# Performance work log

Hardware: AMD Instinct MI355X
Metric: run time of the kernel (lower is better)

The kernel has to match this reference:

```python
import jax, jax.numpy as jnp
import numpy as np


def _conv1x1(x, w, b):
    # x: (B,C,H,W), w: (O,C), b: (O,)
    return jnp.einsum('oc,bchw->bohw', w, x) + b[None, :, None, None]


def _avg_pool2(x):
    B, C, H, W = x.shape
    return x.reshape(B, C, H // 2, 2, W // 2, 2).mean(axis=(3, 5))


def setup_inputs() -> dict:
    key = jax.random.key(0)
    B, C, H, W = 8, 64, 64, 64
    ks = jax.random.split(key, 14)
    s = 1.0 / np.sqrt(C)

    def wb(k1, k2):
        return (jax.random.uniform(k1, (C, C), jnp.float32, -s, s),
                jax.random.uniform(k2, (C,), jnp.float32, -s, s))

    w_q, b_q = wb(ks[0], ks[1])
    w_K, b_K = wb(ks[2], ks[3])
    w_V, b_V = wb(ks[4], ks[5])
    w_Q, b_Q = wb(ks[6], ks[7])
    w_k, b_k = wb(ks[8], ks[9])
    w_v, b_v = wb(ks[10], ks[11])
    x = jax.random.normal(ks[12], (B, C, H, W), jnp.float32)
    gamma = jnp.ones((1,), jnp.float32)
    return dict(x=x, w_q=w_q, b_q=b_q, w_K=w_K, b_K=b_K, w_V=w_V, b_V=b_V,
                w_Q=w_Q, b_Q=b_Q, w_k=w_k, b_k=b_k, w_v=w_v, b_v=b_v,
                gamma=gamma)


def reference(x, w_q, b_q, w_K, b_K, w_V, b_V, w_Q, b_Q, w_k, b_k, w_v, b_v, gamma):
    B, C, H, W = x.shape
    N = H * W
    N4 = N // 4

    # Stage 1: pooled queries vs full key/value
    q = _conv1x1(x, w_q, b_q)                      # (B,C,H,W); torch views as (B,C,W,H) but H==W
    qp = _avg_pool2(q).reshape(B, C, N4).transpose(0, 2, 1)   # (B,N/4,C)
    Kf = _conv1x1(x, w_K, b_K).reshape(B, C, N)                # (B,C,N)
    Vf = _conv1x1(x, w_V, b_V).reshape(B, C, N)                # (B,C,N)
    attn = jax.nn.softmax(jnp.einsum('bnc,bcm->bnm', qp, Kf), axis=-1)  # (B,N/4,N)
    out = jnp.einsum('bcm,bnm->bcn', Vf, attn)                 # (B,C,N/4)
    out = out.reshape(B, C, H // 2, W // 2)

    # Stage 2: full queries vs pooled-derived key/value
    Qf = _conv1x1(x, w_Q, b_Q).reshape(B, C, N).transpose(0, 2, 1)  # (B,N,C)
    kp = _conv1x1(out, w_k, b_k).reshape(B, C, N4)                  # (B,C,N/4)
    vp = _conv1x1(out, w_v, b_v).reshape(B, C, N4)                  # (B,C,N/4)
    attn2 = jax.nn.softmax(jnp.einsum('bnc,bcm->bnm', Qf, kp), axis=-1)  # (B,N,N/4)
    out2 = jnp.einsum('bcm,bnm->bcn', vp, attn2).reshape(B, C, H, W)

    return gamma * out2 + x
```

## Files before the change

kernel.cpp:

```cpp
#include <hip/hip_runtime.h>
#include <math.h>


typedef __bf16 bf16;
typedef __attribute__((ext_vector_type(4))) __bf16 bf16x4;
typedef __attribute__((ext_vector_type(8))) __bf16 bf16x8;
typedef __attribute__((ext_vector_type(4))) float f32x4;

__global__ __launch_bounds__(256) void transpool_kernel(const float* __restrict__ x,
                                                        bf16* __restrict__ xT,
                                                        bf16* __restrict__ xpT) {
    __shared__ float tile[128 * 65];
    const int t  = threadIdx.x;
    const int h2 = blockIdx.x;
    const int b  = blockIdx.y;
    const int n0 = h2 * 128;
    #pragma unroll
    for (int i = 0; i < 32; ++i) {
        int lin = i * 256 + t;
        int n = lin & 127, c = lin >> 7;
        tile[n * 65 + c] = x[((size_t)b * 64 + c) * 4096 + n0 + n];
    }
    __syncthreads();
    #pragma unroll
    for (int i = 0; i < 4; ++i) {
        int slot = i * 256 + t;
        int n = slot >> 3, c0 = (slot & 7) * 8;
        bf16 tmp[8];
        #pragma unroll
        for (int j = 0; j < 8; ++j) tmp[j] = (bf16)tile[n * 65 + c0 + j];
        *(bf16x8*)(xT + ((size_t)b * 4096 + n0 + n) * 64 + c0) = *(bf16x8*)tmp;
    }
    {
        int wp = t & 31, c0 = (t >> 5) * 8;
        bf16 tmp[8];
        #pragma unroll
        for (int j = 0; j < 8; ++j) {
            float a = tile[(2 * wp) * 65 + c0 + j] + tile[(2 * wp + 1) * 65 + c0 + j]
                    + tile[(64 + 2 * wp) * 65 + c0 + j] + tile[(64 + 2 * wp + 1) * 65 + c0 + j];
            tmp[j] = (bf16)(0.25f * a);
        }
        *(bf16x8*)(xpT + ((size_t)b * 1024 + h2 * 32 + wp) * 64 + c0) = *(bf16x8*)tmp;
    }
}

__global__ __launch_bounds__(256) void proj_all_kernel(
    const bf16* __restrict__ xT, const bf16* __restrict__ xpT,
    const float* __restrict__ w_K, const float* __restrict__ b_K, bf16* __restrict__ Kt,
    const float* __restrict__ w_Q, const float* __restrict__ b_Q, bf16* __restrict__ Qt,
    const float* __restrict__ w_V, const float* __restrict__ b_V, bf16* __restrict__ Vf,
    const float* __restrict__ w_q, const float* __restrict__ b_q, bf16* __restrict__ qpt)
{
    const int z = blockIdx.z;
    if (z == 3 && blockIdx.x >= 4) return;
    const bf16*  XT = (z == 3) ? xpT : xT;
    const int    N  = (z == 3) ? 1024 : 4096;
    const float* W  = (z == 0) ? w_K : (z == 1) ? w_Q : (z == 2) ? w_V : w_q;
    const float* Bs = (z == 0) ? b_K : (z == 1) ? b_Q : (z == 2) ? b_V : b_q;
    bf16*        Y  = (z == 0) ? Kt  : (z == 1) ? Qt  : (z == 2) ? Vf  : qpt;
    const int    tr = (z == 2) ? 0 : 1;

    const int lane = threadIdx.x & 63;
    const int w    = threadIdx.x >> 6;
    const int c16 = lane & 15, q4 = lane >> 4;
    const int n0 = (blockIdx.x * 4 + w) * 64;
    const int b  = blockIdx.y;

    bf16x8 wa[4][2];
    #pragma unroll
    for (int to = 0; to < 4; ++to)
        #pragma unroll
        for (int h = 0; h < 2; ++h) {
            const float* wp = W + (16 * to + c16) * 64 + q4 * 8 + 32 * h;
            float4 f0 = *(const float4*)wp;
            float4 f1 = *(const float4*)(wp + 4);
            bf16 tmp[8] = {(bf16)f0.x, (bf16)f0.y, (bf16)f0.z, (bf16)f0.w,
                           (bf16)f1.x, (bf16)f1.y, (bf16)f1.z, (bf16)f1.w};
            wa[to][h] = *(bf16x8*)tmp;
        }

    f32x4 acc[4][4];
    #pragma unroll
    for (int to = 0; to < 4; ++to)
        #pragma unroll
        for (int tn = 0; tn < 4; ++tn) acc[to][tn] = (f32x4){0.f, 0.f, 0.f, 0.f};

    #pragma unroll
    for (int tn = 0; tn < 4; ++tn) {
        const bf16* xrow = XT + ((size_t)b * N + n0 + 16 * tn + c16) * 64 + q4 * 8;
        bf16x8 xb0 = *(const bf16x8*)xrow;
        bf16x8 xb1 = *(const bf16x8*)(xrow + 32);
        #pragma unroll
        for (int to = 0; to < 4; ++to) {
            acc[to][tn] = __builtin_amdgcn_mfma_f32_16x16x32_bf16(wa[to][0], xb0, acc[to][tn], 0, 0, 0);
            acc[to][tn] = __builtin_amdgcn_mfma_f32_16x16x32_bf16(wa[to][1], xb1, acc[to][tn], 0, 0, 0);
        }
    }

    #pragma unroll
    for (int to = 0; to < 4; ++to) {
        float4 b4 = *(const float4*)(Bs + 16 * to + q4 * 4);
        float bias[4] = {b4.x, b4.y, b4.z, b4.w};
        #pragma unroll
        for (int tn = 0; tn < 4; ++tn) {
            if (tr) {
                bf16 yv[4];
                #pragma unroll
                for (int r = 0; r < 4; ++r) yv[r] = (bf16)(acc[to][tn][r] + bias[r]);
                *(bf16x4*)(Y + ((size_t)b * N + n0 + 16 * tn + c16) * 64 + 16 * to + q4 * 4) = *(bf16x4*)yv;
            } else {
                #pragma unroll
                for (int r = 0; r < 4; ++r)
                    Y[((size_t)b * 64 + 16 * to + q4 * 4 + r) * N + n0 + 16 * tn + c16] =
                        (bf16)(acc[to][tn][r] + bias[r]);
            }
        }
    }
}

template<int NSPLIT, int PLAYOUT>
__global__ __launch_bounds__(256) void flash_kernel(
    const bf16* __restrict__ Qt, const bf16* __restrict__ Kt,
    const bf16* __restrict__ Vn, int NQ, int L,
    float* __restrict__ Opart, float* __restrict__ Mbuf, float* __restrict__ Lbuf)
{
    const int tid  = threadIdx.x;
    const int lane = tid & 63;
    const int w    = tid >> 6;
    const int c16  = lane & 15;
    const int q4   = lane >> 4;
    const int b    = blockIdx.y;
    const int n0   = blockIdx.x * 128 + w * 32;
    const int s    = blockIdx.z;
    const int SL   = L / NSPLIT;
    const int k0   = s * SL;
    const int ntiles = SL / 64;

    __shared__ __align__(16) bf16 Ks[2][64 * 72];
    __shared__ __align__(16) bf16 Vs[2][64 * 72];
    __shared__ __align__(16) bf16 Pw[4][32 * 72];

    const int srow = tid >> 2;
    const int scol = (tid & 3) * 16;

    const bf16* Kb = Kt + (size_t)b * L * 64;
    const bf16* Vb = Vn + (size_t)b * 64 * L;

    bf16x8 bq[2][2];
    #pragma unroll
    for (int u = 0; u < 2; ++u) {
        const bf16* qrow = Qt + ((size_t)b * NQ + n0 + 16 * u + c16) * 64 + q4 * 8;
        bq[u][0] = *(const bf16x8*)(qrow);
        bq[u][1] = *(const bf16x8*)(qrow + 32);
    }

    f32x4 O[2][4];
    #pragma unroll
    for (int u = 0; u < 2; ++u)
        #pragma unroll
        for (int g = 0; g < 4; ++g) O[u][g] = (f32x4){0.f, 0.f, 0.f, 0.f};
    float m_run[2] = {-INFINITY, -INFINITY};
    float l_run[2] = {0.f, 0.f};

    {
        const bf16* kg = Kb + ((size_t)(k0 + srow)) * 64 + scol;
        *(bf16x8*)&Ks[0][srow * 72 + scol]     = *(const bf16x8*)kg;
        *(bf16x8*)&Ks[0][srow * 72 + scol + 8] = *(const bf16x8*)(kg + 8);
        const bf16* vg = Vb + (size_t)srow * L + k0 + scol;
        *(bf16x8*)&Vs[0][srow * 72 + scol]     = *(const bf16x8*)vg;
        *(bf16x8*)&Vs[0][srow * 72 + scol + 8] = *(const bf16x8*)(vg + 8);
    }
    __syncthreads();

    for (int it = 0; it < ntiles; ++it) {
        const int buf = it & 1;
        if (it + 1 < ntiles) {
            const int kn = k0 + (it + 1) * 64;
            const bf16* kg = Kb + ((size_t)(kn + srow)) * 64 + scol;
            *(bf16x8*)&Ks[buf ^ 1][srow * 72 + scol]     = *(const bf16x8*)kg;
            *(bf16x8*)&Ks[buf ^ 1][srow * 72 + scol + 8] = *(const bf16x8*)(kg + 8);
            const bf16* vg = Vb + (size_t)srow * L + kn + scol;
            *(bf16x8*)&Vs[buf ^ 1][srow * 72 + scol]     = *(const bf16x8*)vg;
            *(bf16x8*)&Vs[buf ^ 1][srow * 72 + scol + 8] = *(const bf16x8*)(vg + 8);
        }

        f32x4 sv[2][4];
        #pragma unroll
        for (int t = 0; t < 4; ++t) {
            const bf16* krow = &Ks[buf][(16 * t + c16) * 72 + q4 * 8];
            bf16x8 ak0 = *(const bf16x8*)(krow);
            bf16x8 ak1 = *(const bf16x8*)(krow + 32);
            #pragma unroll
            for (int u = 0; u < 2; ++u) {
                f32x4 z = (f32x4){0.f, 0.f, 0.f, 0.f};
                z = __builtin_amdgcn_mfma_f32_16x16x32_bf16(ak0, bq[u][0], z, 0, 0, 0);
                sv[u][t] = __builtin_amdgcn_mfma_f32_16x16x32_bf16(ak1, bq[u][1], z, 0, 0, 0);
            }
        }

        #pragma unroll
        for (int u = 0; u < 2; ++u) {
            float mx = sv[u][0][0];
            #pragma unroll
            for (int t = 0; t < 4; ++t)
                #pragma unroll
                for (int r = 0; r < 4; ++r) mx = fmaxf(mx, sv[u][t][r]);
            mx = fmaxf(mx, __shfl_xor(mx, 16));
            mx = fmaxf(mx, __shfl_xor(mx, 32));
            float nm = fmaxf(m_run[u], mx);
            float alpha = __expf(m_run[u] - nm);
            m_run[u] = nm;

            float ls = 0.f;
            #pragma unroll
            for (int t = 0; t < 4; ++t)
                #pragma unroll
                for (int r = 0; r < 4; ++r) {
                    float p = __expf(sv[u][t][r] - nm);
                    sv[u][t][r] = p;
                    ls += p;
                }
            ls += __shfl_xor(ls, 16);
            ls += __shfl_xor(ls, 32);
            l_run[u] = l_run[u] * alpha + ls;
            #pragma unroll
            for (int g = 0; g < 4; ++g)
                #pragma unroll
                for (int r = 0; r < 4; ++r) O[u][g][r] *= alpha;

            #pragma unroll
            for (int t = 0; t < 4; ++t) {
                bf16x4 pv;
                pv[0] = (bf16)sv[u][t][0]; pv[1] = (bf16)sv[u][t][1];
                pv[2] = (bf16)sv[u][t][2]; pv[3] = (bf16)sv[u][t][3];
                *(bf16x4*)&Pw[w][(16 * u + c16) * 72 + 16 * t + 4 * q4] = pv;
            }
        }

        #pragma unroll
        for (int h = 0; h < 2; ++h) {
            bf16x8 pf0 = *(const bf16x8*)&Pw[w][(c16) * 72 + 32 * h + 8 * q4];
            bf16x8 pf1 = *(const bf16x8*)&Pw[w][(16 + c16) * 72 + 32 * h + 8 * q4];
            #pragma unroll
            for (int g = 0; g < 4; ++g) {
                bf16x8 av = *(const bf16x8*)&Vs[buf][(16 * g + c16) * 72 + 32 * h + q4 * 8];
                O[0][g] = __builtin_amdgcn_mfma_f32_16x16x32_bf16(av, pf0, O[0][g], 0, 0, 0);
                O[1][g] = __builtin_amdgcn_mfma_f32_16x16x32_bf16(av, pf1, O[1][g], 0, 0, 0);
            }
        }
        __syncthreads();
    }

    if (PLAYOUT == 1) {
        #pragma unroll
        for (int u = 0; u < 2; ++u) {
            float* dst = Opart + ((size_t)(b * NSPLIT + s) * NQ + n0 + 16 * u + c16) * 64 + q4 * 4;
            #pragma unroll
            for (int g = 0; g < 4; ++g) *(f32x4*)(dst + 16 * g) = O[u][g];
        }
    } else {
        #pragma unroll
        for (int u = 0; u < 2; ++u)
            #pragma unroll
            for (int g = 0; g < 4; ++g)
                #pragma unroll
                for (int r = 0; r < 4; ++r)
                    Opart[((size_t)(b * NSPLIT + s) * 64 + 16 * g + 4 * q4 + r) * NQ + n0 + 16 * u + c16] = O[u][g][r];
    }
    if (lane < 16) {
        #pragma unroll
        for (int u = 0; u < 2; ++u) {
            Mbuf[(b * NSPLIT + s) * NQ + n0 + 16 * u + lane] = m_run[u];
            Lbuf[(b * NSPLIT + s) * NQ + n0 + 16 * u + lane] = l_run[u];
        }
    }
}

__global__ __launch_bounds__(256) void comb1kv_kernel(
    const float* __restrict__ Opart, const float* __restrict__ Mbuf,
    const float* __restrict__ Lbuf,
    const float* __restrict__ w_k, const float* __restrict__ b_k, bf16* __restrict__ kpt,
    const float* __restrict__ w_v, const float* __restrict__ b_v, bf16* __restrict__ vp)
{
    __shared__ __align__(16) bf16 tile[64 * 72];
    __shared__ float wbuf[64 * 8];
    const int t  = threadIdx.x;
    const int m0 = blockIdx.x * 64;
    const int b  = blockIdx.y;

    if (t < 64) {
        int m = m0 + t;
        float ms[8], ls[8];
        #pragma unroll
        for (int s = 0; s < 8; ++s) {
            ms[s] = Mbuf[(b * 8 + s) * 1024 + m];
            ls[s] = Lbuf[(b * 8 + s) * 1024 + m];
        }
        float M = ms[0];
        #pragma unroll
        for (int s = 1; s < 8; ++s) M = fmaxf(M, ms[s]);
        float wsv[8], lt = 0.f;
        #pragma unroll
        for (int s = 0; s < 8; ++s) { wsv[s] = __expf(ms[s] - M); lt += ls[s] * wsv[s]; }
        float inv = 1.f / lt;
        #pragma unroll
        for (int s = 0; s < 8; ++s) wbuf[t * 8 + s] = wsv[s] * inv;
    }
    __syncthreads();

    #pragma unroll
    for (int i = 0; i < 4; ++i) {
        int ml = i * 16 + (t >> 4);
        int c4 = (t & 15) * 4;
        const float* base = Opart + ((size_t)(b * 8) * 1024 + m0 + ml) * 64 + c4;
        float a0 = 0.f, a1 = 0.f, a2 = 0.f, a3 = 0.f;
        #pragma unroll
        for (int s = 0; s < 8; ++s) {
            f32x4 v = *(const f32x4*)(base + (size_t)s * 1024 * 64);
            float wg = wbuf[ml * 8 + s];
            a0 += v[0] * wg; a1 += v[1] * wg; a2 += v[2] * wg; a3 += v[3] * wg;
        }
        bf16x4 o; o[0] = (bf16)a0; o[1] = (bf16)a1; o[2] = (bf16)a2; o[3] = (bf16)a3;
        *(bf16x4*)&tile[ml * 72 + c4] = o;
    }
    __syncthreads();

    const int lane = t & 63;
    const int w    = t >> 6;
    const int c16 = lane & 15, q4 = lane >> 4;

    if (w < 2) {
        bf16x8 wb[4][2];
        #pragma unroll
        for (int to = 0; to < 4; ++to)
            #pragma unroll
            for (int h = 0; h < 2; ++h) {
                const float* wp = w_k + (16 * to + c16) * 64 + q4 * 8 + 32 * h;
                float4 f0 = *(const float4*)wp;
                float4 f1 = *(const float4*)(wp + 4);
                bf16 tmp[8] = {(bf16)f0.x, (bf16)f0.y, (bf16)f0.z, (bf16)f0.w,
                               (bf16)f1.x, (bf16)f1.y, (bf16)f1.z, (bf16)f1.w};
                wb[to][h] = *(bf16x8*)tmp;
            }
        #pragma unroll
        for (int tm2 = 0; tm2 < 2; ++tm2) {
            int tm = w * 2 + tm2;
            bf16x8 a0 = *(const bf16x8*)&tile[(16 * tm + c16) * 72 + q4 * 8];
            bf16x8 a1 = *(const bf16x8*)&tile[(16 * tm + c16) * 72 + q4 * 8 + 32];
            #pragma unroll
            for (int to = 0; to < 4; ++to) {
                f32x4 acc = (f32x4){0.f, 0.f, 0.f, 0.f};
                acc = __builtin_amdgcn_mfma_f32_16x16x32_bf16(a0, wb[to][0], acc, 0, 0, 0);
                acc = __builtin_amdgcn_mfma_f32_16x16x32_bf16(a1, wb[to][1], acc, 0, 0, 0);
                float bias = b_k[16 * to + c16];
                #pragma unroll
                for (int r = 0; r < 4; ++r)
                    kpt[((size_t)b * 1024 + m0 + 16 * tm + 4 * q4 + r) * 64 + 16 * to + c16] =
                        (bf16)(acc[r] + bias);
            }
        }
    } else {
        bf16x8 wa[4][2];
        #pragma unroll
        for (int ta = 0; ta < 4; ++ta)
            #pragma unroll
            for (int h = 0; h < 2; ++h) {
                const float* wp = w_v + (16 * ta + c16) * 64 + q4 * 8 + 32 * h;
                float4 f0 = *(const float4*)wp;
                float4 f1 = *(const float4*)(wp + 4);
                bf16 tmp[8] = {(bf16)f0.x, (bf16)f0.y, (bf16)f0.z, (bf16)f0.w,
                               (bf16)f1.x, (bf16)f1.y, (bf16)f1.z, (bf16)f1.w};
                wa[ta][h] = *(bf16x8*)tmp;
            }
        #pragma unroll
        for (int tm2 = 0; tm2 < 2; ++tm2) {
            int tm = (w - 2) * 2 + tm2;
            bf16x8 bb0 = *(const bf16x8*)&tile[(16 * tm + c16) * 72 + q4 * 8];
            bf16x8 bb1 = *(const bf16x8*)&tile[(16 * tm + c16) * 72 + q4 * 8 + 32];
            #pragma unroll
            for (int ta = 0; ta < 4; ++ta) {
                f32x4 acc = (f32x4){0.f, 0.f, 0.f, 0.f};
                acc = __builtin_amdgcn_mfma_f32_16x16x32_bf16(wa[ta][0], bb0, acc, 0, 0, 0);
                acc = __builtin_amdgcn_mfma_f32_16x16x32_bf16(wa[ta][1], bb1, acc, 0, 0, 0);
                float4 b4 = *(const float4*)(b_v + 16 * ta + 4 * q4);
                float bias[4] = {b4.x, b4.y, b4.z, b4.w};
                #pragma unroll
                for (int r = 0; r < 4; ++r)
                    vp[((size_t)b * 64 + 16 * ta + 4 * q4 + r) * 1024 + m0 + 16 * tm + c16] =
                        (bf16)(acc[r] + bias[r]);
            }
        }
    }
}

__global__ __launch_bounds__(256) void combine2_kernel(
    const float* __restrict__ Opart, const float* __restrict__ Mbuf,
    const float* __restrict__ Lbuf, const float* __restrict__ x,
    const float* __restrict__ gamma_p, float* __restrict__ out)
{
    int idx = blockIdx.x * 256 + threadIdx.x;
    int n = idx & 4095;
    int b = idx >> 18;
    float m0 = Mbuf[(b * 2 + 0) * 4096 + n], m1 = Mbuf[(b * 2 + 1) * 4096 + n];
    float l0 = Lbuf[(b * 2 + 0) * 4096 + n], l1 = Lbuf[(b * 2 + 1) * 4096 + n];
    float M = fmaxf(m0, m1);
    float w0 = __expf(m0 - M), w1 = __expf(m1 - M);
    float lt = l0 * w0 + l1 * w1;
    int c = (idx >> 12) & 63;
    float acc = Opart[((size_t)(b * 2 + 0) * 64 + c) * 4096 + n] * w0
              + Opart[((size_t)(b * 2 + 1) * 64 + c) * 4096 + n] * w1;
    out[idx] = gamma_p[0] * (acc / lt) + x[idx];
}

extern "C" void kernel_launch(void* const* d_in, const int* in_sizes, int n_in,
                              void* d_out, int out_size, void* d_ws, size_t ws_size,
                              hipStream_t stream) {
    const float* x    = (const float*)d_in[0];
    const float* w_q  = (const float*)d_in[1];
    const float* b_q  = (const float*)d_in[2];
    const float* w_K  = (const float*)d_in[3];
    const float* b_K  = (const float*)d_in[4];
    const float* w_V  = (const float*)d_in[5];
    const float* b_V  = (const float*)d_in[6];
    const float* w_Q  = (const float*)d_in[7];
    const float* b_Q  = (const float*)d_in[8];
    const float* w_k  = (const float*)d_in[9];
    const float* b_k  = (const float*)d_in[10];
    const float* w_v  = (const float*)d_in[11];
    const float* b_v  = (const float*)d_in[12];
    const float* gamma = (const float*)d_in[13];
    float* out = (float*)d_out;

    char* ws = (char*)d_ws;
    bf16*  xT    = (bf16*)ws;   ws += (size_t)8 * 4096 * 64 * 2;
    bf16*  Kt    = (bf16*)ws;   ws += (size_t)8 * 4096 * 64 * 2;
    bf16*  Qt    = (bf16*)ws;   ws += (size_t)8 * 4096 * 64 * 2;
    bf16*  Vf    = (bf16*)ws;   ws += (size_t)8 * 4096 * 64 * 2;
    bf16*  xpT   = (bf16*)ws;   ws += (size_t)8 * 1024 * 64 * 2;
    bf16*  qpt   = (bf16*)ws;   ws += (size_t)8 * 1024 * 64 * 2;
    bf16*  kpt   = (bf16*)ws;   ws += (size_t)8 * 1024 * 64 * 2;
    bf16*  vp    = (bf16*)ws;   ws += (size_t)8 * 64 * 1024 * 2;
    float* Opart = (float*)ws;  ws += (size_t)8 * 8 * 1024 * 64 * 4;
    float* Mb    = (float*)ws;  ws += (size_t)8 * 8 * 1024 * 4;
    float* Lb    = (float*)ws;  ws += (size_t)8 * 8 * 1024 * 4;

    transpool_kernel<<<dim3(32, 8), 256, 0, stream>>>(x, xT, xpT);

    proj_all_kernel<<<dim3(16, 8, 4), 256, 0, stream>>>(
        xT, xpT, w_K, b_K, Kt, w_Q, b_Q, Qt, w_V, b_V, Vf, w_q, b_q, qpt);

    flash_kernel<8, 1><<<dim3(8, 8, 8), 256, 0, stream>>>(
        qpt, Kt, Vf, 1024, 4096, Opart, Mb, Lb);

    comb1kv_kernel<<<dim3(16, 8), 256, 0, stream>>>(
        Opart, Mb, Lb, w_k, b_k, kpt, w_v, b_v, vp);

    flash_kernel<2, 0><<<dim3(32, 8, 2), 256, 0, stream>>>(
        Qt, kpt, vp, 4096, 1024, Opart, Mb, Lb);

    combine2_kernel<<<8192, 256, 0, stream>>>(Opart, Mb, Lb, x, gamma, out);
}
```

Baseline: 163.5 us.

## Raise split-K counts, store normalized bf16 partials, pass P via lane shuffles

Doubles the key-split count in both flash-attention stages (16 and 4 splits) so the grid has more blocks. Each split now normalizes its partial output by its own row sum and writes it as bf16, halving partial-buffer traffic. The combine kernels are updated to weight by l·exp(m−M). The P matrix is no longer round-tripped through shared memory; it is packed into registers and rearranged with cross-lane shuffles into the MFMA B-operand layout. The trade-offs are extra combine reads per split, added shuffle work, and lower precision in the stored partials.

```diff
diff --git a/kernel.cpp b/kernel.cpp
--- a/kernel.cpp
+++ b/kernel.cpp
@@ -3,9 +3,17 @@
 
 
 typedef __bf16 bf16;
+typedef __attribute__((ext_vector_type(2))) __bf16 bf16x2;
 typedef __attribute__((ext_vector_type(4))) __bf16 bf16x4;
 typedef __attribute__((ext_vector_type(8))) __bf16 bf16x8;
 typedef __attribute__((ext_vector_type(4))) float f32x4;
+
+union Pack2 { unsigned int u; bf16x2 v; };
+union PackU { unsigned int u[4]; bf16x8 v; };
+
+__device__ inline unsigned int pack_bf16(float a, float b) {
+    Pack2 p; p.v = (bf16x2){(bf16)a, (bf16)b}; return p.u;
+}
 
 __global__ __launch_bounds__(256) void transpool_kernel(const float* __restrict__ x,
                                                         bf16* __restrict__ xT,
@@ -122,7 +130,7 @@
 __global__ __launch_bounds__(256) void flash_kernel(
     const bf16* __restrict__ Qt, const bf16* __restrict__ Kt,
     const bf16* __restrict__ Vn, int NQ, int L,
-    float* __restrict__ Opart, float* __restrict__ Mbuf, float* __restrict__ Lbuf)
+    bf16* __restrict__ Opart, float* __restrict__ Mbuf, float* __restrict__ Lbuf)
 {
     const int tid  = threadIdx.x;
     const int lane = tid & 63;
@@ -138,10 +146,13 @@
 
     __shared__ __align__(16) bf16 Ks[2][64 * 72];
     __shared__ __align__(16) bf16 Vs[2][64 * 72];
-    __shared__ __align__(16) bf16 Pw[4][32 * 72];
 
     const int srow = tid >> 2;
     const int scol = (tid & 3) * 16;
+
+    const int lane_a = c16 | (((2 * q4) & 3) << 4);
+    const int lane_b = c16 | (((2 * q4 + 1) & 3) << 4);
+    const bool hi = (q4 >= 2);
 
     const bf16* Kb = Kt + (size_t)b * L * 64;
     const bf16* Vb = Vn + (size_t)b * 64 * L;
@@ -198,6 +209,7 @@
             }
         }
 
+        unsigned int pk[2][4][2];
         #pragma unroll
         for (int u = 0; u < 2; ++u) {
             float mx = sv[u][0][0];
@@ -230,42 +242,61 @@
 
             #pragma unroll
             for (int t = 0; t < 4; ++t) {
-                bf16x4 pv;
-                pv[0] = (bf16)sv[u][t][0]; pv[1] = (bf16)sv[u][t][1];
-                pv[2] = (bf16)sv[u][t][2]; pv[3] = (bf16)sv[u][t][3];
-                *(bf16x4*)&Pw[w][(16 * u + c16) * 72 + 16 * t + 4 * q4] = pv;
+                pk[u][t][0] = pack_bf16(sv[u][t][0], sv[u][t][1]);
+                pk[u][t][1] = pack_bf16(sv[u][t][2], sv[u][t][3]);
             }
         }
 
         #pragma unroll
         for (int h = 0; h < 2; ++h) {
-            bf16x8 pf0 = *(const bf16x8*)&Pw[w][(c16) * 72 + 32 * h + 8 * q4];
-            bf16x8 pf1 = *(const bf16x8*)&Pw[w][(16 + c16) * 72 + 32 * h + 8 * q4];
+            bf16x8 pf[2];
+            #pragma unroll
+            for (int u = 0; u < 2; ++u) {
+                unsigned xa0 = __shfl((int)pk[u][2 * h][0], lane_a);
+                unsigned xa1 = __shfl((int)pk[u][2 * h][1], lane_a);
+                unsigned ya0 = __shfl((int)pk[u][2 * h + 1][0], lane_a);
+                unsigned ya1 = __shfl((int)pk[u][2 * h + 1][1], lane_a);
+                unsigned xb0 = __shfl((int)pk[u][2 * h][0], lane_b);
+                unsigned xb1 = __shfl((int)pk[u][2 * h][1], lane_b);
+                unsigned yb0 = __shfl((int)pk[u][2 * h + 1][0], lane_b);
+                unsigned yb1 = __shfl((int)pk[u][2 * h + 1][1], lane_b);
+                PackU pu;
+                pu.u[0] = hi ? ya0 : xa0;
+                pu.u[1] = hi ? ya1 : xa1;
+                pu.u[2] = hi ? yb0 : xb0;
+                pu.u[3] = hi ? yb1 : xb1;
+                pf[u] = pu.v;
+            }
             #pragma unroll
             for (int g = 0; g < 4; ++g) {
                 bf16x8 av = *(const bf16x8*)&Vs[buf][(16 * g + c16) * 72 + 32 * h + q4 * 8];
-                O[0][g] = __builtin_amdgcn_mfma_f32_16x16x32_bf16(av, pf0, O[0][g], 0, 0, 0);
-                O[1][g] = __builtin_amdgcn_mfma_f32_16x16x32_bf16(av, pf1, O[1][g], 0, 0, 0);
+                O[0][g] = __builtin_amdgcn_mfma_f32_16x16x32_bf16(av, pf[0], O[0][g], 0, 0, 0);
+                O[1][g] = __builtin_amdgcn_mfma_f32_16x16x32_bf16(av, pf[1], O[1][g], 0, 0, 0);
             }
         }
         __syncthreads();
     }
 
-    if (PLAYOUT == 1) {
-        #pragma unroll
-        for (int u = 0; u < 2; ++u) {
-            float* dst = Opart + ((size_t)(b * NSPLIT + s) * NQ + n0 + 16 * u + c16) * 64 + q4 * 4;
-            #pragma unroll
-            for (int g = 0; g < 4; ++g) *(f32x4*)(dst + 16 * g) = O[u][g];
-        }
-    } else {
-        #pragma unroll
-        for (int u = 0; u < 2; ++u)
+    #pragma unroll
+    for (int u = 0; u < 2; ++u) {
+        float inv = 1.0f / l_run[u];
+        if (PLAYOUT == 1) {
+            bf16* dst = Opart + ((size_t)(b * NSPLIT + s) * NQ + n0 + 16 * u + c16) * 64 + q4 * 4;
+            #pragma unroll
+            for (int g = 0; g < 4; ++g) {
+                bf16x4 yv;
+                #pragma unroll
+                for (int r = 0; r < 4; ++r) yv[r] = (bf16)(O[u][g][r] * inv);
+                *(bf16x4*)(dst + 16 * g) = yv;
+            }
+        } else {
             #pragma unroll
             for (int g = 0; g < 4; ++g)
                 #pragma unroll
                 for (int r = 0; r < 4; ++r)
-                    Opart[((size_t)(b * NSPLIT + s) * 64 + 16 * g + 4 * q4 + r) * NQ + n0 + 16 * u + c16] = O[u][g][r];
+                    Opart[((size_t)(b * NSPLIT + s) * 64 + 16 * g + 4 * q4 + r) * NQ + n0 + 16 * u + c16] =
+                        (bf16)(O[u][g][r] * inv);
+        }
     }
     if (lane < 16) {
         #pragma unroll
@@ -277,34 +308,34 @@
 }
 
 __global__ __launch_bounds__(256) void comb1kv_kernel(
-    const float* __restrict__ Opart, const float* __restrict__ Mbuf,
+    const bf16* __restrict__ Opart, const float* __restrict__ Mbuf,
     const float* __restrict__ Lbuf,
     const float* __restrict__ w_k, const float* __restrict__ b_k, bf16* __restrict__ kpt,
     const float* __restrict__ w_v, const float* __restrict__ b_v, bf16* __restrict__ vp)
 {
     __shared__ __align__(16) bf16 tile[64 * 72];
-    __shared__ float wbuf[64 * 8];
+    __shared__ float wbuf[64 * 16];
     const int t  = threadIdx.x;
     const int m0 = blockIdx.x * 64;
     const int b  = blockIdx.y;
 
     if (t < 64) {
         int m = m0 + t;
-        float ms[8], ls[8];
-        #pragma unroll
-        for (int s = 0; s < 8; ++s) {
-            ms[s] = Mbuf[(b * 8 + s) * 1024 + m];
-            ls[s] = Lbuf[(b * 8 + s) * 1024 + m];
+        float ms[16], ls[16];
+        #pragma unroll
+        for (int s = 0; s < 16; ++s) {
+            ms[s] = Mbuf[(b * 16 + s) * 1024 + m];
+            ls[s] = Lbuf[(b * 16 + s) * 1024 + m];
         }
         float M = ms[0];
         #pragma unroll
-        for (int s = 1; s < 8; ++s) M = fmaxf(M, ms[s]);
-        float wsv[8], lt = 0.f;
-        #pragma unroll
-        for (int s = 0; s < 8; ++s) { wsv[s] = __expf(ms[s] - M); lt += ls[s] * wsv[s]; }
+        for (int s = 1; s < 16; ++s) M = fmaxf(M, ms[s]);
+        float wsv[16], lt = 0.f;
+        #pragma unroll
+        for (int s = 0; s < 16; ++s) { wsv[s] = ls[s] * __expf(ms[s] - M); lt += wsv[s]; }
         float inv = 1.f / lt;
         #pragma unroll
-        for (int s = 0; s < 8; ++s) wbuf[t * 8 + s] = wsv[s] * inv;
+        for (int s = 0; s < 16; ++s) wbuf[t * 16 + s] = wsv[s] * inv;
     }
     __syncthreads();
 
@@ -312,13 +343,14 @@
     for (int i = 0; i < 4; ++i) {
         int ml = i * 16 + (t >> 4);
         int c4 = (t & 15) * 4;
-        const float* base = Opart + ((size_t)(b * 8) * 1024 + m0 + ml) * 64 + c4;
+        const bf16* base = Opart + ((size_t)(b * 16) * 1024 + m0 + ml) * 64 + c4;
         float a0 = 0.f, a1 = 0.f, a2 = 0.f, a3 = 0.f;
         #pragma unroll
-        for (int s = 0; s < 8; ++s) {
-            f32x4 v = *(const f32x4*)(base + (size_t)s * 1024 * 64);
-            float wg = wbuf[ml * 8 + s];
-            a0 += v[0] * wg; a1 += v[1] * wg; a2 += v[2] * wg; a3 += v[3] * wg;
+        for (int s = 0; s < 16; ++s) {
+            bf16x4 v = *(const bf16x4*)(base + (size_t)s * 1024 * 64);
+            float wg = wbuf[ml * 16 + s];
+            a0 += (float)v[0] * wg; a1 += (float)v[1] * wg;
+            a2 += (float)v[2] * wg; a3 += (float)v[3] * wg;
         }
         bf16x4 o; o[0] = (bf16)a0; o[1] = (bf16)a1; o[2] = (bf16)a2; o[3] = (bf16)a3;
         *(bf16x4*)&tile[ml * 72 + c4] = o;
@@ -394,21 +426,28 @@
 }
 
 __global__ __launch_bounds__(256) void combine2_kernel(
-    const float* __restrict__ Opart, const float* __restrict__ Mbuf,
+    const bf16* __restrict__ Opart, const float* __restrict__ Mbuf,
     const float* __restrict__ Lbuf, const float* __restrict__ x,
     const float* __restrict__ gamma_p, float* __restrict__ out)
 {
     int idx = blockIdx.x * 256 + threadIdx.x;
     int n = idx & 4095;
     int b = idx >> 18;
-    float m0 = Mbuf[(b * 2 + 0) * 4096 + n], m1 = Mbuf[(b * 2 + 1) * 4096 + n];
-    float l0 = Lbuf[(b * 2 + 0) * 4096 + n], l1 = Lbuf[(b * 2 + 1) * 4096 + n];
-    float M = fmaxf(m0, m1);
-    float w0 = __expf(m0 - M), w1 = __expf(m1 - M);
-    float lt = l0 * w0 + l1 * w1;
     int c = (idx >> 12) & 63;
-    float acc = Opart[((size_t)(b * 2 + 0) * 64 + c) * 4096 + n] * w0
-              + Opart[((size_t)(b * 2 + 1) * 64 + c) * 4096 + n] * w1;
+    float ms[4], ls[4];
+    #pragma unroll
+    for (int s = 0; s < 4; ++s) {
+        ms[s] = Mbuf[(b * 4 + s) * 4096 + n];
+        ls[s] = Lbuf[(b * 4 + s) * 4096 + n];
+    }
+    float M = fmaxf(fmaxf(ms[0], ms[1]), fmaxf(ms[2], ms[3]));
+    float lt = 0.f, acc = 0.f;
+    #pragma unroll
+    for (int s = 0; s < 4; ++s) {
+        float wg = ls[s] * __expf(ms[s] - M);
+        lt += wg;
+        acc += (float)Opart[((size_t)(b * 4 + s) * 64 + c) * 4096 + n] * wg;
+    }
     out[idx] = gamma_p[0] * (acc / lt) + x[idx];
 }
 
@@ -440,22 +479,22 @@
     bf16*  qpt   = (bf16*)ws;   ws += (size_t)8 * 1024 * 64 * 2;
     bf16*  kpt   = (bf16*)ws;   ws += (size_t)8 * 1024 * 64 * 2;
     bf16*  vp    = (bf16*)ws;   ws += (size_t)8 * 64 * 1024 * 2;
-    float* Opart = (float*)ws;  ws += (size_t)8 * 8 * 1024 * 64 * 4;
-    float* Mb    = (float*)ws;  ws += (size_t)8 * 8 * 1024 * 4;
-    float* Lb    = (float*)ws;  ws += (size_t)8 * 8 * 1024 * 4;
+    bf16*  Opart = (bf16*)ws;   ws += (size_t)8 * 16 * 1024 * 64 * 2;
+    float* Mb    = (float*)ws;  ws += (size_t)8 * 16 * 1024 * 4;
+    float* Lb    = (float*)ws;  ws += (size_t)8 * 16 * 1024 * 4;
 
     transpool_kernel<<<dim3(32, 8), 256, 0, stream>>>(x, xT, xpT);
 
     proj_all_kernel<<<dim3(16, 8, 4), 256, 0, stream>>>(
         xT, xpT, w_K, b_K, Kt, w_Q, b_Q, Qt, w_V, b_V, Vf, w_q, b_q, qpt);
 
-    flash_kernel<8, 1><<<dim3(8, 8, 8), 256, 0, stream>>>(
+    flash_kernel<16, 1><<<dim3(8, 8, 16), 256, 0, stream>>>(
         qpt, Kt, Vf, 1024, 4096, Opart, Mb, Lb);
 
     comb1kv_kernel<<<dim3(16, 8), 256, 0, stream>>>(
         Opart, Mb, Lb, w_k, b_k, kpt, w_v, b_v, vp);
 
-    flash_kernel<2, 0><<<dim3(32, 8, 2), 256, 0, stream>>>(
+    flash_kernel<4, 0><<<dim3(32, 8, 4), 256, 0, stream>>>(
         Qt, kpt, vp, 4096, 1024, Opart, Mb, Lb);
 
     combine2_kernel<<<8192, 256, 0, stream>>>(Opart, Mb, Lb, x, gamma, out);
```

After: 164.8 us. No clear change (+0.8%).

## Fuse transpose/pool with projections and store normalized split outputs in bf16

Applied to the files above, without the earlier changes.

Merges the transpose/pooling kernel with the four 1x1 projection GEMMs, so x is staged in shared memory as bf16 and projected directly, dropping the xT/xpT global round trip and one launch. Flash partial outputs are now normalized by their own row sum and stored as bf16 rather than fp32, halving partial-output traffic; the combine kernels reweight with l*exp(m-M). The comb1kv grid is doubled with half-size tiles for more parallelism. The prep grid stays at 256 blocks doing serial per-wave GEMM work, and bf16 partials reduce precision.

```diff
diff --git a/kernel.cpp b/kernel.cpp
--- a/kernel.cpp
+++ b/kernel.cpp
@@ -7,65 +7,12 @@
 typedef __attribute__((ext_vector_type(8))) __bf16 bf16x8;
 typedef __attribute__((ext_vector_type(4))) float f32x4;
 
-__global__ __launch_bounds__(256) void transpool_kernel(const float* __restrict__ x,
-                                                        bf16* __restrict__ xT,
-                                                        bf16* __restrict__ xpT) {
-    __shared__ float tile[128 * 65];
-    const int t  = threadIdx.x;
-    const int h2 = blockIdx.x;
-    const int b  = blockIdx.y;
-    const int n0 = h2 * 128;
-    #pragma unroll
-    for (int i = 0; i < 32; ++i) {
-        int lin = i * 256 + t;
-        int n = lin & 127, c = lin >> 7;
-        tile[n * 65 + c] = x[((size_t)b * 64 + c) * 4096 + n0 + n];
-    }
-    __syncthreads();
-    #pragma unroll
-    for (int i = 0; i < 4; ++i) {
-        int slot = i * 256 + t;
-        int n = slot >> 3, c0 = (slot & 7) * 8;
-        bf16 tmp[8];
-        #pragma unroll
-        for (int j = 0; j < 8; ++j) tmp[j] = (bf16)tile[n * 65 + c0 + j];
-        *(bf16x8*)(xT + ((size_t)b * 4096 + n0 + n) * 64 + c0) = *(bf16x8*)tmp;
-    }
-    {
-        int wp = t & 31, c0 = (t >> 5) * 8;
-        bf16 tmp[8];
-        #pragma unroll
-        for (int j = 0; j < 8; ++j) {
-            float a = tile[(2 * wp) * 65 + c0 + j] + tile[(2 * wp + 1) * 65 + c0 + j]
-                    + tile[(64 + 2 * wp) * 65 + c0 + j] + tile[(64 + 2 * wp + 1) * 65 + c0 + j];
-            tmp[j] = (bf16)(0.25f * a);
-        }
-        *(bf16x8*)(xpT + ((size_t)b * 1024 + h2 * 32 + wp) * 64 + c0) = *(bf16x8*)tmp;
-    }
-}
-
-__global__ __launch_bounds__(256) void proj_all_kernel(
-    const bf16* __restrict__ xT, const bf16* __restrict__ xpT,
-    const float* __restrict__ w_K, const float* __restrict__ b_K, bf16* __restrict__ Kt,
-    const float* __restrict__ w_Q, const float* __restrict__ b_Q, bf16* __restrict__ Qt,
-    const float* __restrict__ w_V, const float* __restrict__ b_V, bf16* __restrict__ Vf,
-    const float* __restrict__ w_q, const float* __restrict__ b_q, bf16* __restrict__ qpt)
+__device__ __forceinline__ void proj_wave(
+    const bf16* __restrict__ src, int TN,
+    const float* __restrict__ W, const float* __restrict__ Bs,
+    bf16* __restrict__ Y, int tr, int N, int b, int gn0, int lane)
 {
-    const int z = blockIdx.z;
-    if (z == 3 && blockIdx.x >= 4) return;
-    const bf16*  XT = (z == 3) ? xpT : xT;
-    const int    N  = (z == 3) ? 1024 : 4096;
-    const float* W  = (z == 0) ? w_K : (z == 1) ? w_Q : (z == 2) ? w_V : w_q;
-    const float* Bs = (z == 0) ? b_K : (z == 1) ? b_Q : (z == 2) ? b_V : b_q;
-    bf16*        Y  = (z == 0) ? Kt  : (z == 1) ? Qt  : (z == 2) ? Vf  : qpt;
-    const int    tr = (z == 2) ? 0 : 1;
-
-    const int lane = threadIdx.x & 63;
-    const int w    = threadIdx.x >> 6;
     const int c16 = lane & 15, q4 = lane >> 4;
-    const int n0 = (blockIdx.x * 4 + w) * 64;
-    const int b  = blockIdx.y;
-
     bf16x8 wa[4][2];
     #pragma unroll
     for (int to = 0; to < 4; ++to)
@@ -78,43 +25,89 @@
                            (bf16)f1.x, (bf16)f1.y, (bf16)f1.z, (bf16)f1.w};
             wa[to][h] = *(bf16x8*)tmp;
         }
-
-    f32x4 acc[4][4];
-    #pragma unroll
-    for (int to = 0; to < 4; ++to)
-        #pragma unroll
-        for (int tn = 0; tn < 4; ++tn) acc[to][tn] = (f32x4){0.f, 0.f, 0.f, 0.f};
-
-    #pragma unroll
-    for (int tn = 0; tn < 4; ++tn) {
-        const bf16* xrow = XT + ((size_t)b * N + n0 + 16 * tn + c16) * 64 + q4 * 8;
-        bf16x8 xb0 = *(const bf16x8*)xrow;
-        bf16x8 xb1 = *(const bf16x8*)(xrow + 32);
+    for (int tn = 0; tn < TN; ++tn) {
+        bf16x8 xb0 = *(const bf16x8*)&src[(16 * tn + c16) * 72 + q4 * 8];
+        bf16x8 xb1 = *(const bf16x8*)&src[(16 * tn + c16) * 72 + q4 * 8 + 32];
         #pragma unroll
         for (int to = 0; to < 4; ++to) {
-            acc[to][tn] = __builtin_amdgcn_mfma_f32_16x16x32_bf16(wa[to][0], xb0, acc[to][tn], 0, 0, 0);
-            acc[to][tn] = __builtin_amdgcn_mfma_f32_16x16x32_bf16(wa[to][1], xb1, acc[to][tn], 0, 0, 0);
-        }
-    }
-
-    #pragma unroll
-    for (int to = 0; to < 4; ++to) {
-        float4 b4 = *(const float4*)(Bs + 16 * to + q4 * 4);
-        float bias[4] = {b4.x, b4.y, b4.z, b4.w};
-        #pragma unroll
-        for (int tn = 0; tn < 4; ++tn) {
+            f32x4 acc = (f32x4){0.f, 0.f, 0.f, 0.f};
+            acc = __builtin_amdgcn_mfma_f32_16x16x32_bf16(wa[to][0], xb0, acc, 0, 0, 0);
+            acc = __builtin_amdgcn_mfma_f32_16x16x32_bf16(wa[to][1], xb1, acc, 0, 0, 0);
             if (tr) {
-                bf16 yv[4];
-                #pragma unroll
-                for (int r = 0; r < 4; ++r) yv[r] = (bf16)(acc[to][tn][r] + bias[r]);
-                *(bf16x4*)(Y + ((size_t)b * N + n0 + 16 * tn + c16) * 64 + 16 * to + q4 * 4) = *(bf16x4*)yv;
+                float4 b4 = *(const float4*)(Bs + 16 * to + q4 * 4);
+                bf16x4 yv;
+                yv[0] = (bf16)(acc[0] + b4.x); yv[1] = (bf16)(acc[1] + b4.y);
+                yv[2] = (bf16)(acc[2] + b4.z); yv[3] = (bf16)(acc[3] + b4.w);
+                *(bf16x4*)(Y + ((size_t)b * N + gn0 + 16 * tn + c16) * 64 + 16 * to + q4 * 4) = yv;
             } else {
+                float4 b4 = *(const float4*)(Bs + 16 * to + q4 * 4);
+                float bias[4] = {b4.x, b4.y, b4.z, b4.w};
                 #pragma unroll
                 for (int r = 0; r < 4; ++r)
-                    Y[((size_t)b * 64 + 16 * to + q4 * 4 + r) * N + n0 + 16 * tn + c16] =
-                        (bf16)(acc[to][tn][r] + bias[r]);
-            }
-        }
+                    Y[((size_t)b * 64 + 16 * to + q4 * 4 + r) * N + gn0 + 16 * tn + c16] =
+                        (bf16)(acc[r] + bias[r]);
+            }
+        }
+    }
+}
+
+__global__ __launch_bounds__(256) void prep_kernel(
+    const float* __restrict__ x,
+    const float* __restrict__ w_K, const float* __restrict__ b_K, bf16* __restrict__ Kt,
+    const float* __restrict__ w_Q, const float* __restrict__ b_Q, bf16* __restrict__ Qt,
+    const float* __restrict__ w_V, const float* __restrict__ b_V, bf16* __restrict__ Vf,
+    const float* __restrict__ w_q, const float* __restrict__ b_q, bf16* __restrict__ qpt)
+{
+    __shared__ float tile[128 * 65];
+    __shared__ __align__(16) bf16 xbT[128 * 72];
+    __shared__ __align__(16) bf16 xpb[32 * 72];
+    const int t  = threadIdx.x;
+    const int h2 = blockIdx.x;
+    const int b  = blockIdx.y;
+    const int n0 = h2 * 128;
+
+    #pragma unroll
+    for (int i = 0; i < 32; ++i) {
+        int lin = i * 256 + t;
+        int n = lin & 127, c = lin >> 7;
+        tile[n * 65 + c] = x[((size_t)b * 64 + c) * 4096 + n0 + n];
+    }
+    __syncthreads();
+    #pragma unroll
+    for (int i = 0; i < 4; ++i) {
+        int slot = i * 256 + t;
+        int n = slot >> 3, c0 = (slot & 7) * 8;
+        bf16 tmp[8];
+        #pragma unroll
+        for (int j = 0; j < 8; ++j) tmp[j] = (bf16)tile[n * 65 + c0 + j];
+        *(bf16x8*)&xbT[n * 72 + c0] = *(bf16x8*)tmp;
+    }
+    {
+        int wp = t & 31, c0 = (t >> 5) * 8;
+        bf16 tmp[8];
+        #pragma unroll
+        for (int j = 0; j < 8; ++j) {
+            float a = tile[(2 * wp) * 65 + c0 + j] + tile[(2 * wp + 1) * 65 + c0 + j]
+                    + tile[(64 + 2 * wp) * 65 + c0 + j] + tile[(64 + 2 * wp + 1) * 65 + c0 + j];
+            tmp[j] = (bf16)(0.25f * a);
+        }
+        *(bf16x8*)&xpb[wp * 72 + c0] = *(bf16x8*)tmp;
+    }
+    __syncthreads();
+
+    const int lane = t & 63;
+    const int w    = t >> 6;
+    {
+        const int mat  = w >> 1;
+        const int half = w & 1;
+        proj_wave(xbT + half * 64 * 72, 4,
+                  mat == 0 ? w_K : w_Q, mat == 0 ? b_K : b_Q,
+                  mat == 0 ? Kt : Qt, 1, 4096, b, n0 + half * 64, lane);
+    }
+    if (w < 2) {
+        proj_wave(xbT + w * 64 * 72, 4, w_V, b_V, Vf, 0, 4096, b, n0 + w * 64, lane);
+    } else if (w == 2) {
+        proj_wave(xpb, 2, w_q, b_q, qpt, 1, 1024, b, h2 * 32, lane);
     }
 }
 
@@ -122,7 +115,7 @@
 __global__ __launch_bounds__(256) void flash_kernel(
     const bf16* __restrict__ Qt, const bf16* __restrict__ Kt,
     const bf16* __restrict__ Vn, int NQ, int L,
-    float* __restrict__ Opart, float* __restrict__ Mbuf, float* __restrict__ Lbuf)
+    bf16* __restrict__ Opart, float* __restrict__ Mbuf, float* __restrict__ Lbuf)
 {
     const int tid  = threadIdx.x;
     const int lane = tid & 63;
@@ -251,21 +244,26 @@
         __syncthreads();
     }
 
-    if (PLAYOUT == 1) {
-        #pragma unroll
-        for (int u = 0; u < 2; ++u) {
-            float* dst = Opart + ((size_t)(b * NSPLIT + s) * NQ + n0 + 16 * u + c16) * 64 + q4 * 4;
-            #pragma unroll
-            for (int g = 0; g < 4; ++g) *(f32x4*)(dst + 16 * g) = O[u][g];
-        }
-    } else {
-        #pragma unroll
-        for (int u = 0; u < 2; ++u)
+    #pragma unroll
+    for (int u = 0; u < 2; ++u) {
+        float inv = 1.0f / l_run[u];
+        if (PLAYOUT == 1) {
+            bf16* dst = Opart + ((size_t)(b * NSPLIT + s) * NQ + n0 + 16 * u + c16) * 64 + q4 * 4;
+            #pragma unroll
+            for (int g = 0; g < 4; ++g) {
+                bf16x4 yv;
+                #pragma unroll
+                for (int r = 0; r < 4; ++r) yv[r] = (bf16)(O[u][g][r] * inv);
+                *(bf16x4*)(dst + 16 * g) = yv;
+            }
+        } else {
             #pragma unroll
             for (int g = 0; g < 4; ++g)
                 #pragma unroll
                 for (int r = 0; r < 4; ++r)
-                    Opart[((size_t)(b * NSPLIT + s) * 64 + 16 * g + 4 * q4 + r) * NQ + n0 + 16 * u + c16] = O[u][g][r];
+                    Opart[((size_t)(b * NSPLIT + s) * 64 + 16 * g + 4 * q4 + r) * NQ + n0 + 16 * u + c16] =
+                        (bf16)(O[u][g][r] * inv);
+        }
     }
     if (lane < 16) {
         #pragma unroll
@@ -277,18 +275,18 @@
 }
 
 __global__ __launch_bounds__(256) void comb1kv_kernel(
-    const float* __restrict__ Opart, const float* __restrict__ Mbuf,
+    const bf16* __restrict__ Opart, const float* __restrict__ Mbuf,
     const float* __restrict__ Lbuf,
     const float* __restrict__ w_k, const float* __restrict__ b_k, bf16* __restrict__ kpt,
     const float* __restrict__ w_v, const float* __restrict__ b_v, bf16* __restrict__ vp)
 {
-    __shared__ __align__(16) bf16 tile[64 * 72];
-    __shared__ float wbuf[64 * 8];
+    __shared__ __align__(16) bf16 tile[32 * 72];
+    __shared__ float wbuf[32 * 8];
     const int t  = threadIdx.x;
-    const int m0 = blockIdx.x * 64;
+    const int m0 = blockIdx.x * 32;
     const int b  = blockIdx.y;
 
-    if (t < 64) {
+    if (t < 32) {
         int m = m0 + t;
         float ms[8], ls[8];
         #pragma unroll
@@ -301,7 +299,7 @@
         for (int s = 1; s < 8; ++s) M = fmaxf(M, ms[s]);
         float wsv[8], lt = 0.f;
         #pragma unroll
-        for (int s = 0; s < 8; ++s) { wsv[s] = __expf(ms[s] - M); lt += ls[s] * wsv[s]; }
+        for (int s = 0; s < 8; ++s) { wsv[s] = ls[s] * __expf(ms[s] - M); lt += wsv[s]; }
         float inv = 1.f / lt;
         #pragma unroll
         for (int s = 0; s < 8; ++s) wbuf[t * 8 + s] = wsv[s] * inv;
@@ -309,16 +307,17 @@
     __syncthreads();
 
     #pragma unroll
-    for (int i = 0; i < 4; ++i) {
+    for (int i = 0; i < 2; ++i) {
         int ml = i * 16 + (t >> 4);
         int c4 = (t & 15) * 4;
-        const float* base = Opart + ((size_t)(b * 8) * 1024 + m0 + ml) * 64 + c4;
+        const bf16* base = Opart + ((size_t)(b * 8) * 1024 + m0 + ml) * 64 + c4;
         float a0 = 0.f, a1 = 0.f, a2 = 0.f, a3 = 0.f;
         #pragma unroll
         for (int s = 0; s < 8; ++s) {
-            f32x4 v = *(const f32x4*)(base + (size_t)s * 1024 * 64);
+            bf16x4 v = *(const bf16x4*)(base + (size_t)s * 1024 * 64);
             float wg = wbuf[ml * 8 + s];
-            a0 += v[0] * wg; a1 += v[1] * wg; a2 += v[2] * wg; a3 += v[3] * wg;
+            a0 += (float)v[0] * wg; a1 += (float)v[1] * wg;
+            a2 += (float)v[2] * wg; a3 += (float)v[3] * wg;
         }
         bf16x4 o; o[0] = (bf16)a0; o[1] = (bf16)a1; o[2] = (bf16)a2; o[3] = (bf16)a3;
         *(bf16x4*)&tile[ml * 72 + c4] = o;
@@ -342,22 +341,19 @@
                                (bf16)f1.x, (bf16)f1.y, (bf16)f1.z, (bf16)f1.w};
                 wb[to][h] = *(bf16x8*)tmp;
             }
-        #pragma unroll
-        for (int tm2 = 0; tm2 < 2; ++tm2) {
-            int tm = w * 2 + tm2;
-            bf16x8 a0 = *(const bf16x8*)&tile[(16 * tm + c16) * 72 + q4 * 8];
-            bf16x8 a1 = *(const bf16x8*)&tile[(16 * tm + c16) * 72 + q4 * 8 + 32];
-            #pragma unroll
-            for (int to = 0; to < 4; ++to) {
-                f32x4 acc = (f32x4){0.f, 0.f, 0.f, 0.f};
-                acc = __builtin_amdgcn_mfma_f32_16x16x32_bf16(a0, wb[to][0], acc, 0, 0, 0);
-                acc = __builtin_amdgcn_mfma_f32_16x16x32_bf16(a1, wb[to][1], acc, 0, 0, 0);
-                float bias = b_k[16 * to + c16];
-                #pragma unroll
-                for (int r = 0; r < 4; ++r)
-                    kpt[((size_t)b * 1024 + m0 + 16 * tm + 4 * q4 + r) * 64 + 16 * to + c16] =
-                        (bf16)(acc[r] + bias);
-            }
+        const int tm = w;
+        bf16x8 a0 = *(const bf16x8*)&tile[(16 * tm + c16) * 72 + q4 * 8];
+        bf16x8 a1 = *(const bf16x8*)&tile[(16 * tm + c16) * 72 + q4 * 8 + 32];
+        #pragma unroll
+        for (int to = 0; to < 4; ++to) {
+            f32x4 acc = (f32x4){0.f, 0.f, 0.f, 0.f};
+            acc = __builtin_amdgcn_mfma_f32_16x16x32_bf16(a0, wb[to][0], acc, 0, 0, 0);
+            acc = __builtin_amdgcn_mfma_f32_16x16x32_bf16(a1, wb[to][1], acc, 0, 0, 0);
+            float bias = b_k[16 * to + c16];
+            #pragma unroll
+            for (int r = 0; r < 4; ++r)
+                kpt[((size_t)b * 1024 + m0 + 16 * tm + 4 * q4 + r) * 64 + 16 * to + c16] =
+                    (bf16)(acc[r] + bias);
         }
     } else {
         bf16x8 wa[4][2];
@@ -372,44 +368,40 @@
                                (bf16)f1.x, (bf16)f1.y, (bf16)f1.z, (bf16)f1.w};
                 wa[ta][h] = *(bf16x8*)tmp;
             }
-        #pragma unroll
-        for (int tm2 = 0; tm2 < 2; ++tm2) {
-            int tm = (w - 2) * 2 + tm2;
-            bf16x8 bb0 = *(const bf16x8*)&tile[(16 * tm + c16) * 72 + q4 * 8];
-            bf16x8 bb1 = *(const bf16x8*)&tile[(16 * tm + c16) * 72 + q4 * 8 + 32];
-            #pragma unroll
-            for (int ta = 0; ta < 4; ++ta) {
-                f32x4 acc = (f32x4){0.f, 0.f, 0.f, 0.f};
-                acc = __builtin_amdgcn_mfma_f32_16x16x32_bf16(wa[ta][0], bb0, acc, 0, 0, 0);
-                acc = __builtin_amdgcn_mfma_f32_16x16x32_bf16(wa[ta][1], bb1, acc, 0, 0, 0);
-                float4 b4 = *(const float4*)(b_v + 16 * ta + 4 * q4);
-                float bias[4] = {b4.x, b4.y, b4.z, b4.w};
-                #pragma unroll
-                for (int r = 0; r < 4; ++r)
-                    vp[((size_t)b * 64 + 16 * ta + 4 * q4 + r) * 1024 + m0 + 16 * tm + c16] =
-                        (bf16)(acc[r] + bias[r]);
-            }
+        const int tm = w - 2;
+        bf16x8 bb0 = *(const bf16x8*)&tile[(16 * tm + c16) * 72 + q4 * 8];
+        bf16x8 bb1 = *(const bf16x8*)&tile[(16 * tm + c16) * 72 + q4 * 8 + 32];
+        #pragma unroll
+        for (int ta = 0; ta < 4; ++ta) {
+            f32x4 acc = (f32x4){0.f, 0.f, 0.f, 0.f};
+            acc = __builtin_amdgcn_mfma_f32_16x16x32_bf16(wa[ta][0], bb0, acc, 0, 0, 0);
+            acc = __builtin_amdgcn_mfma_f32_16x16x32_bf16(wa[ta][1], bb1, acc, 0, 0, 0);
+            float4 b4 = *(const float4*)(b_v + 16 * ta + 4 * q4);
+            float bias[4] = {b4.x, b4.y, b4.z, b4.w};
+            #pragma unroll
+            for (int r = 0; r < 4; ++r)
+                vp[((size_t)b * 64 + 16 * ta + 4 * q4 + r) * 1024 + m0 + 16 * tm + c16] =
+                    (bf16)(acc[r] + bias[r]);
         }
     }
 }
 
 __global__ __launch_bounds__(256) void combine2_kernel(
-    const float* __restrict__ Opart, const float* __restrict__ Mbuf,
+    const bf16* __restrict__ Opart, const float* __restrict__ Mbuf,
     const float* __restrict__ Lbuf, const float* __restrict__ x,
     const float* __restrict__ gamma_p, float* __restrict__ out)
 {
     int idx = blockIdx.x * 256 + threadIdx.x;
     int n = idx & 4095;
     int b = idx >> 18;
+    int c = (idx >> 12) & 63;
     float m0 = Mbuf[(b * 2 + 0) * 4096 + n], m1 = Mbuf[(b * 2 + 1) * 4096 + n];
     float l0 = Lbuf[(b * 2 + 0) * 4096 + n], l1 = Lbuf[(b * 2 + 1) * 4096 + n];
     float M = fmaxf(m0, m1);
-    float w0 = __expf(m0 - M), w1 = __expf(m1 - M);
-    float lt = l0 * w0 + l1 * w1;
-    int c = (idx >> 12) & 63;
-    float acc = Opart[((size_t)(b * 2 + 0) * 64 + c) * 4096 + n] * w0
-              + Opart[((size_t)(b * 2 + 1) * 64 + c) * 4096 + n] * w1;
-    out[idx] = gamma_p[0] * (acc / lt) + x[idx];
+    float w0 = l0 * __expf(m0 - M), w1 = l1 * __expf(m1 - M);
+    float acc = (float)Opart[((size_t)(b * 2 + 0) * 64 + c) * 4096 + n] * w0
+              + (float)Opart[((size_t)(b * 2 + 1) * 64 + c) * 4096 + n] * w1;
+    out[idx] = gamma_p[0] * (acc / (w0 + w1)) + x[idx];
 }
 
 extern "C" void kernel_launch(void* const* d_in, const int* in_sizes, int n_in,
@@ -432,27 +424,23 @@
     float* out = (float*)d_out;
 
     char* ws = (char*)d_ws;
-    bf16*  xT    = (bf16*)ws;   ws += (size_t)8 * 4096 * 64 * 2;
     bf16*  Kt    = (bf16*)ws;   ws += (size_t)8 * 4096 * 64 * 2;
     bf16*  Qt    = (bf16*)ws;   ws += (size_t)8 * 4096 * 64 * 2;
     bf16*  Vf    = (bf16*)ws;   ws += (size_t)8 * 4096 * 64 * 2;
-    bf16*  xpT   = (bf16*)ws;   ws += (size_t)8 * 1024 * 64 * 2;
     bf16*  qpt   = (bf16*)ws;   ws += (size_t)8 * 1024 * 64 * 2;
     bf16*  kpt   = (bf16*)ws;   ws += (size_t)8 * 1024 * 64 * 2;
     bf16*  vp    = (bf16*)ws;   ws += (size_t)8 * 64 * 1024 * 2;
-    float* Opart = (float*)ws;  ws += (size_t)8 * 8 * 1024 * 64 * 4;
+    bf16*  Opart = (bf16*)ws;   ws += (size_t)8 * 8 * 1024 * 64 * 2;
     float* Mb    = (float*)ws;  ws += (size_t)8 * 8 * 1024 * 4;
     float* Lb    = (float*)ws;  ws += (size_t)8 * 8 * 1024 * 4;
 
-    transpool_kernel<<<dim3(32, 8), 256, 0, stream>>>(x, xT, xpT);
-
-    proj_all_kernel<<<dim3(16, 8, 4), 256, 0, stream>>>(
-        xT, xpT, w_K, b_K, Kt, w_Q, b_Q, Qt, w_V, b_V, Vf, w_q, b_q, qpt);
+    prep_kernel<<<dim3(32, 8), 256, 0, stream>>>(
+        x, w_K, b_K, Kt, w_Q, b_Q, Qt, w_V, b_V, Vf, w_q, b_q, qpt);
 
     flash_kernel<8, 1><<<dim3(8, 8, 8), 256, 0, stream>>>(
         qpt, Kt, Vf, 1024, 4096, Opart, Mb, Lb);
 
-    comb1kv_kernel<<<dim3(16, 8), 256, 0, stream>>>(
+    comb1kv_kernel<<<dim3(32, 8), 256, 0, stream>>>(
         Opart, Mb, Lb, w_k, b_k, kpt, w_v, b_v, vp);
 
     flash_kernel<2, 0><<<dim3(32, 8, 2), 256, 0, stream>>>(
```

After: 150.2 us. 8.1% less time.
